# Performance work log

Hardware: AMD Instinct MI355X
Metric: run time of the kernel (lower is better)

Reference implementation:

```python
import jax, jax.numpy as jnp
import numpy as np

HIDDEN = 2048
N_HEADS = 16
HEAD_DIM = HIDDEN // N_HEADS  # 128
GROUP_SIZE = 128
ROPE_THETA = 10000.0
EPS = 1e-8
THRESH = 0.5


def ternary_quantize_groupwise(w):
    O, I = w.shape
    wg = w.reshape(O, I // GROUP_SIZE, GROUP_SIZE)
    scale = jnp.maximum(jnp.mean(jnp.abs(wg), axis=-1, keepdims=True), EPS)
    wn = wg / scale
    q = jnp.where(wn > THRESH, 1.0, jnp.where(wn < -THRESH, -1.0, 0.0))
    return (q * scale).reshape(O, I)


def quantize_with_ste(w):
    wq = ternary_quantize_groupwise(w)
    return w + jax.lax.stop_gradient(wq - w)


def rope_tables(seqlen):
    half = HEAD_DIM // 2
    inv_freq = 1.0 / (ROPE_THETA ** (jnp.arange(half, dtype=jnp.float32) / half))
    freqs = jnp.arange(seqlen, dtype=jnp.float32)[:, None] * inv_freq[None, :]  # [S, half]
    return jnp.cos(freqs), jnp.sin(freqs)


def apply_rope(x, cos, sin):
    # x: [B, H, S, D]; cos/sin: [S, D/2]
    d = x.shape[-1]
    x1, x2 = x[..., : d // 2], x[..., d // 2:]
    c = cos[None, None, :, :].astype(x.dtype)
    s = sin[None, None, :, :].astype(x.dtype)
    return jnp.concatenate([x1 * c - x2 * s, x1 * s + x2 * c], axis=-1)


def setup_inputs() -> dict:
    key = jax.random.key(0)
    ks = jax.random.split(key, 5)
    B, S = 1, 2048
    hidden_states = jax.random.normal(ks[0], (B, S, HIDDEN), dtype=jnp.float32)
    attention_mask = jnp.ones((B, S), dtype=jnp.int32)
    init_scale = 1.0 / np.sqrt(HIDDEN)
    wq = jax.random.normal(ks[1], (HIDDEN, HIDDEN), dtype=jnp.float32) * init_scale
    wk = jax.random.normal(ks[2], (HIDDEN, HIDDEN), dtype=jnp.float32) * init_scale
    wv = jax.random.normal(ks[3], (HIDDEN, HIDDEN), dtype=jnp.float32) * init_scale
    wo = jax.random.normal(ks[4], (HIDDEN, HIDDEN), dtype=jnp.float32) * init_scale
    return {"hidden_states": hidden_states, "attention_mask": attention_mask,
            "wq": wq, "wk": wk, "wv": wv, "wo": wo}


def reference(hidden_states, attention_mask, wq, wk, wv, wo):
    B, S, _ = hidden_states.shape
    cos, sin = rope_tables(S)

    def proj(x, w):
        w_q = quantize_with_ste(w)
        y = jnp.einsum('bsi,oi->bso', x, w_q)
        return y.reshape(B, S, N_HEADS, HEAD_DIM).transpose(0, 2, 1, 3)  # [B,H,S,D]

    q = apply_rope(proj(hidden_states, wq), cos, sin)
    k = apply_rope(proj(hidden_states, wk), cos, sin)
    v = proj(hidden_states, wv)

    scores = jnp.einsum('bhsd,bhtd->bhst', q, k) / np.sqrt(HEAD_DIM)
    causal = jnp.triu(jnp.ones((S, S), dtype=bool), k=1)
    scores = jnp.where(causal[None, None, :, :], -jnp.inf, scores)
    pad = (attention_mask == 0)[:, None, None, :]
    scores = jnp.where(pad, -jnp.inf, scores)

    probs = jax.nn.softmax(scores, axis=-1)
    out = jnp.einsum('bhst,bhtd->bhsd', probs, v)
    out = out.transpose(0, 2, 1, 3).reshape(B, S, HIDDEN)

    wo_q = quantize_with_ste(wo)
    return jnp.einsum('bso,po->bsp', out, wo_q)
```

## Files before the change

kernel.cpp:

```cpp
#include <hip/hip_runtime.h>
#include <cstdint>
#include <cstddef>


typedef __attribute__((ext_vector_type(8))) short bf16x8;
typedef __attribute__((ext_vector_type(4))) float f32x4;
typedef __attribute__((address_space(3))) void lds_void;
typedef const __attribute__((address_space(1))) void gmem_void;

__device__ __forceinline__ short f2bf(float x) {
    union { float f; uint32_t u; } c; c.f = x;
    uint32_t r = (c.u + 0x7FFFu + ((c.u >> 16) & 1u)) >> 16;
    return (short)r;
}
__device__ __forceinline__ float bf2f(short x) {
    union { uint32_t u; float f; } c; c.u = ((uint32_t)(uint16_t)x) << 16;
    return c.f;
}

__global__ __launch_bounds__(64) void zero_flag(int* f) {
    if (threadIdx.x == 0) *f = 0;
}

__global__ __launch_bounds__(256) void detect_kernel(
    const unsigned short* __restrict__ p, int n, int* __restrict__ flag)
{
    int tid = blockIdx.x * 256 + threadIdx.x;
    int cnt = 0;
    for (int i = tid; i < n; i += 65536) {
        int e = (p[i] >> 7) & 0xFF;
        cnt += (e >= 0xF0) ? 1 : 0;
    }
#pragma unroll
    for (int off = 1; off < 64; off <<= 1) cnt += __shfl_xor(cnt, off);
    if ((threadIdx.x & 63) == 0 && cnt) atomicAdd(flag, cnt);
}

__global__ __launch_bounds__(256) void convert_kernel(
    const void* __restrict__ in, short* __restrict__ out, int n,
    const int* __restrict__ flag)
{
    bool isf32 = (*flag > 1000);
    int i = (blockIdx.x * 256 + threadIdx.x) * 4;
    if (i >= n) return;
    if (isf32) {
        float4 v = *(const float4*)((const float*)in + i);
        short4 o;
        o.x = f2bf(v.x); o.y = f2bf(v.y); o.z = f2bf(v.z); o.w = f2bf(v.w);
        *(short4*)(out + i) = o;
    } else {
        *(short4*)(out + i) = *(const short4*)((const short*)in + i);
    }
}

__global__ __launch_bounds__(256) void quant_kernel(
    const void* __restrict__ w0, const void* __restrict__ w1,
    const void* __restrict__ w2, const void* __restrict__ w3,
    short* __restrict__ q0, short* __restrict__ q1,
    short* __restrict__ q2, short* __restrict__ q3,
    const int* __restrict__ flag)
{
    bool isf32 = (*flag > 1000);
    int t   = blockIdx.x * 256 + threadIdx.x;
    int mat = t >> 20;
    int e4  = t & 1048575;
    const void* w = (mat == 0) ? w0 : (mat == 1) ? w1 : (mat == 2) ? w2 : w3;
    short*      q = (mat == 0) ? q0 : (mat == 1) ? q1 : (mat == 2) ? q2 : q3;
    float a0, a1, a2, a3;
    if (isf32) {
        float4 v = *(const float4*)((const float*)w + (long long)e4 * 4);
        a0 = v.x; a1 = v.y; a2 = v.z; a3 = v.w;
    } else {
        short4 v = *(const short4*)((const short*)w + (long long)e4 * 4);
        a0 = bf2f(v.x); a1 = bf2f(v.y); a2 = bf2f(v.z); a3 = bf2f(v.w);
    }
    float s = fabsf(a0) + fabsf(a1) + fabsf(a2) + fabsf(a3);
#pragma unroll
    for (int off = 1; off < 32; off <<= 1) s += __shfl_xor(s, off);
    float scale = fmaxf(s * (1.0f / 128.0f), 1e-8f);
    float inv = 1.0f / scale;
    auto qz = [&](float a) -> short {
        float na = a * inv;
        return f2bf((na > 0.5f) ? scale : (na < -0.5f) ? -scale : 0.0f);
    };
    short4 o;
    o.x = qz(a0); o.y = qz(a1); o.z = qz(a2); o.w = qz(a3);
    *(short4*)(q + (long long)e4 * 4) = o;
}

__global__ __launch_bounds__(256, 2) void gemm_qkv(
    const short* __restrict__ A, const short* __restrict__ B,
    short* __restrict__ C)
{
    __shared__ short lds[30720];

    int wg = blockIdx.y * 32 + blockIdx.x;
    int sw = (wg & 7) * 64 + (wg >> 3);
    int bx = sw >> 4, by = sw & 15;

    const short* Ab = A + (long long)by * 128 * 2048;
    const short* Bb = B + (long long)bx * 192 * 2048;

    int tid = threadIdx.x, lane = tid & 63, wid = tid >> 6;
    int wr = wid >> 1, wc = wid & 1;
    int quad = lane >> 4, lm = lane & 15;

    f32x4 acc[4][6];
#pragma unroll
    for (int i = 0; i < 4; i++)
#pragma unroll
        for (int j = 0; j < 6; j++)
#pragma unroll
            for (int r = 0; r < 4; r++) acc[i][j][r] = 0.0f;

    auto stage = [&](int tn, short* buf) {
        short* dA = buf;
        short* dB = buf + 4096;
#pragma unroll
        for (int l = 0; l < 2; l++) {
            int ci  = l * 256 + tid;
            int row = ci >> 2;
            int kc  = ((ci & 3) - (row >> 1)) & 3;
            const short* gp = Ab + (long long)row * 2048 + tn * 32 + kc * 8;
            __builtin_amdgcn_global_load_lds((gmem_void*)gp, (lds_void*)(dA + ci * 8), 16, 0, 0);
        }
#pragma unroll
        for (int l = 0; l < 3; l++) {
            int ci  = l * 256 + tid;
            int row = ci >> 2;
            int kc  = ((ci & 3) - (row >> 1)) & 3;
            const short* gp = Bb + (long long)row * 2048 + tn * 32 + kc * 8;
            __builtin_amdgcn_global_load_lds((gmem_void*)gp, (lds_void*)(dB + ci * 8), 16, 0, 0);
        }
    };

    auto tile = [&](short* cur, short* nxt, int tn, bool pf) {
        if (pf) stage(tn, nxt);
        short* cA = cur;
        short* cB = cur + 4096;
        bf16x8 af[4], bg[6];
#pragma unroll
        for (int m = 0; m < 4; m++) {
            int R = wr * 64 + m * 16 + lm;
            af[m] = *(const bf16x8*)(cA + R * 32 + (((quad + (R >> 1)) & 3) << 3));
        }
#pragma unroll
        for (int n = 0; n < 3; n++) {
            int R = wc * 96 + n * 16 + lm;
            bg[n] = *(const bf16x8*)(cB + R * 32 + (((quad + (R >> 1)) & 3) << 3));
        }
        __builtin_amdgcn_s_setprio(1);
#pragma unroll
        for (int m = 0; m < 4; m++)
#pragma unroll
            for (int n = 0; n < 3; n++)
                acc[m][n] = __builtin_amdgcn_mfma_f32_16x16x32_bf16(af[m], bg[n], acc[m][n], 0, 0, 0);
        __builtin_amdgcn_s_setprio(0);
#pragma unroll
        for (int n = 3; n < 6; n++) {
            int R = wc * 96 + n * 16 + lm;
            bg[n] = *(const bf16x8*)(cB + R * 32 + (((quad + (R >> 1)) & 3) << 3));
        }
        __builtin_amdgcn_s_setprio(1);
#pragma unroll
        for (int m = 0; m < 4; m++)
#pragma unroll
            for (int n = 3; n < 6; n++)
                acc[m][n] = __builtin_amdgcn_mfma_f32_16x16x32_bf16(af[m], bg[n], acc[m][n], 0, 0, 0);
        __builtin_amdgcn_s_setprio(0);
        if (pf) asm volatile("s_waitcnt vmcnt(5)" ::: "memory");
        else    asm volatile("s_waitcnt vmcnt(0)" ::: "memory");
        __builtin_amdgcn_s_barrier();
    };

    short* c0 = lds;
    short* c1 = lds + 10240;
    short* c2 = lds + 20480;
    stage(0, c0);
    stage(1, c1);
    asm volatile("s_waitcnt vmcnt(5)" ::: "memory");
    __builtin_amdgcn_s_barrier();

    for (int t = 0; t < 64; t++) {
        tile(c0, c2, t + 2, t + 2 < 64);
        short* tmp = c0; c0 = c1; c1 = c2; c2 = tmp;
    }

#pragma unroll
    for (int m = 0; m < 4; m++)
#pragma unroll
        for (int n = 0; n < 6; n++)
#pragma unroll
            for (int r = 0; r < 4; r++) {
                int row = by * 128 + wr * 64 + m * 16 + quad * 4 + r;
                int col = bx * 192 + wc * 96 + n * 16 + lm;
                C[(long long)row * 6144 + col] = f2bf(acc[m][n][r]);
            }
}

__global__ __launch_bounds__(256) void ropetrans_kernel(
    const short* __restrict__ qkv,
    short* __restrict__ qr, short* __restrict__ kr,
    short* __restrict__ v_t)
{
    __shared__ short lt[4096];
    int bid = blockIdx.x;
    int tid = threadIdx.x;
    if (bid < 1024) {
        const float QSC = 0.1275174150637756f;
        int idx = bid * 256 + tid;
        int d8 = (idx & 7) * 8;
        int h  = (idx >> 3) & 15;
        int s  = idx >> 7;
        long long io = (long long)s * 6144 + h * 128 + d8;
        long long oo = (long long)h * 262144 + (long long)s * 128 + d8;
        bf16x8 x1q = *(const bf16x8*)(qkv + io);
        bf16x8 x2q = *(const bf16x8*)(qkv + io + 64);
        bf16x8 x1k = *(const bf16x8*)(qkv + io + 2048);
        bf16x8 x2k = *(const bf16x8*)(qkv + io + 2112);
        bf16x8 o1q, o2q, o1k, o2k;
#pragma unroll
        for (int j = 0; j < 8; j++) {
            float inv = exp2f((float)(d8 + j) * -0.20762050593261719f);
            float ang = (float)s * inv;
            float sn, c;
            sincosf(ang, &sn, &c);
            float a1 = bf2f(x1q[j]), a2 = bf2f(x2q[j]);
            o1q[j] = f2bf((a1 * c - a2 * sn) * QSC);
            o2q[j] = f2bf((a1 * sn + a2 * c) * QSC);
            float b1 = bf2f(x1k[j]), b2 = bf2f(x2k[j]);
            o1k[j] = f2bf(b1 * c - b2 * sn);
            o2k[j] = f2bf(b1 * sn + b2 * c);
        }
        *(bf16x8*)(qr + oo)      = o1q;
        *(bf16x8*)(qr + oo + 64) = o2q;
        *(bf16x8*)(kr + oo)      = o1k;
        *(bf16x8*)(kr + oo + 64) = o2k;
    } else {
        int bt = (bid - 1024) & 31, bo = (bid - 1024) >> 5;
        int r = tid >> 3, c = tid & 7;
#pragma unroll
        for (int h = 0; h < 2; h++) {
            int row = h * 32 + r;
            bf16x8 v = *(const bf16x8*)(qkv + (long long)(bt * 64 + row) * 6144 + 4096 + bo * 64 + c * 8);
            *(bf16x8*)(lt + row * 64 + ((c ^ (row & 7)) << 3)) = v;
        }
        __syncthreads();
#pragma unroll
        for (int h = 0; h < 2; h++) {
            int o = h * 32 + r;
            bf16x8 ov;
#pragma unroll
            for (int k = 0; k < 8; k++) {
                int row = c * 8 + k;
                ov[k] = lt[row * 64 + ((((o >> 3) ^ (row & 7))) << 3) + (o & 7)];
            }
            *(bf16x8*)(v_t + (long long)(bo * 64 + o) * 2048 + bt * 64 + c * 8) = ov;
        }
    }
}

__global__ __launch_bounds__(256, 2) void gemm_wo(
    const short* __restrict__ A, const short* __restrict__ B,
    float* __restrict__ C)
{
    __shared__ short lds[18432];

    int wg = blockIdx.y * 32 + blockIdx.x;
    int sw = (wg & 7) * 64 + (wg >> 3);
    int bx = sw & 31, by = sw >> 5;

    const short* Ab = A + (long long)by * 128 * 2048;
    const short* Bb = B + (long long)bx * 64 * 2048;

    int tid = threadIdx.x, lane = tid & 63, wid = tid >> 6;
    int wr = wid >> 1, wc = wid & 1;
    int quad = lane >> 4, lm = lane & 15;

    f32x4 acc[4][2];
#pragma unroll
    for (int i = 0; i < 4; i++)
#pragma unroll
        for (int j = 0; j < 2; j++)
#pragma unroll
            for (int r = 0; r < 4; r++) acc[i][j][r] = 0.0f;

    auto stage = [&](int tn, short* buf) {
        short* dA = buf;
        short* dB = buf + 4096;
#pragma unroll
        for (int l = 0; l < 2; l++) {
            int ci  = l * 256 + tid;
            int row = ci >> 2;
            int kc  = ((ci & 3) - (row >> 1)) & 3;
            const short* gp = Ab + (long long)row * 2048 + tn * 32 + kc * 8;
            __builtin_amdgcn_global_load_lds((gmem_void*)gp, (lds_void*)(dA + ci * 8), 16, 0, 0);
        }
        {
            int ci  = tid;
            int row = ci >> 2;
            int kc  = ((ci & 3) - (row >> 1)) & 3;
            const short* gp = Bb + (long long)row * 2048 + tn * 32 + kc * 8;
            __builtin_amdgcn_global_load_lds((gmem_void*)gp, (lds_void*)(dB + ci * 8), 16, 0, 0);
        }
    };

    auto tile = [&](short* cur, short* nxt, int tn, bool pf) {
        if (pf) stage(tn, nxt);
        short* cA = cur;
        short* cB = cur + 4096;
        bf16x8 af[4], bg[2];
#pragma unroll
        for (int m = 0; m < 4; m++) {
            int R = wr * 64 + m * 16 + lm;
            af[m] = *(const bf16x8*)(cA + R * 32 + (((quad + (R >> 1)) & 3) << 3));
        }
#pragma unroll
        for (int n = 0; n < 2; n++) {
            int R = wc * 32 + n * 16 + lm;
            bg[n] = *(const bf16x8*)(cB + R * 32 + (((quad + (R >> 1)) & 3) << 3));
        }
        __builtin_amdgcn_s_setprio(1);
#pragma unroll
        for (int m = 0; m < 4; m++)
#pragma unroll
            for (int n = 0; n < 2; n++)
                acc[m][n] = __builtin_amdgcn_mfma_f32_16x16x32_bf16(af[m], bg[n], acc[m][n], 0, 0, 0);
        __builtin_amdgcn_s_setprio(0);
        if (pf) asm volatile("s_waitcnt vmcnt(3)" ::: "memory");
        else    asm volatile("s_waitcnt vmcnt(0)" ::: "memory");
        __builtin_amdgcn_s_barrier();
    };

    short* c0 = lds;
    short* c1 = lds + 6144;
    short* c2 = lds + 12288;
    stage(0, c0);
    stage(1, c1);
    asm volatile("s_waitcnt vmcnt(3)" ::: "memory");
    __builtin_amdgcn_s_barrier();

    for (int t = 0; t < 64; t++) {
        tile(c0, c2, t + 2, t + 2 < 64);
        short* tmp = c0; c0 = c1; c1 = c2; c2 = tmp;
    }

#pragma unroll
    for (int m = 0; m < 4; m++)
#pragma unroll
        for (int n = 0; n < 2; n++)
#pragma unroll
            for (int r = 0; r < 4; r++) {
                int row = by * 128 + wr * 64 + m * 16 + quad * 4 + r;
                int col = bx * 64 + wc * 32 + n * 16 + lm;
                C[(long long)row * 2048 + col] = acc[m][n][r];
            }
}

__global__ __launch_bounds__(256) void flash_kernel(
    const short* __restrict__ q_r, const short* __restrict__ k_r,
    const short* __restrict__ v_t, float* __restrict__ Opart,
    float* __restrict__ mpart, float* __restrict__ lpart)
{
    const float THR = 11.5f;
    int bid = blockIdx.x;
    int p = bid >> 5;
    int h = (bid >> 1) & 15;
    int z = bid & 1;

    int tid = threadIdx.x, lane = tid & 63, wv = tid >> 6;
    int quad = lane >> 4, lm = lane & 15;

    __shared__ short lK[64 * 128];
    __shared__ short lV[128 * 64];
    __shared__ short lP[64 * 64];

    const short* kb = k_r + h * 262144;
    const short* vb = v_t + h * 128 * 2048;

    for (int leg = 0; leg < 2; leg++) {
        int qt = leg ? p : 31 - p;
        int n  = qt + 1;
        int jhalf = (n + 1) >> 1;
        int jb = z ? jhalf : 0;
        int je = z ? n : jhalf;

        const short* qb = q_r + h * 262144 + (qt * 64 + wv * 16) * 128;
        bf16x8 aq[4];
#pragma unroll
        for (int kc = 0; kc < 4; kc++)
            aq[kc] = *(const bf16x8*)(qb + lm * 128 + kc * 32 + quad * 8);

        f32x4 ao[8];
#pragma unroll
        for (int nt = 0; nt < 8; nt++)
#pragma unroll
            for (int r = 0; r < 4; r++) ao[nt][r] = 0.0f;
        float mrow[4], lrow[4];
#pragma unroll
        for (int r = 0; r < 4; r++) { mrow[r] = -1e30f; lrow[r] = 0.0f; }

        if (jb < je) {
#pragma unroll
            for (int i = 0; i < 4; i++) {
                int ci = i * 256 + tid;
                int r = ci >> 4, cp = ci & 15;
                int c = (cp & 8) | ((cp & 7) ^ (r & 7));
                const short* gp = kb + (jb * 64 + r) * 128 + c * 8;
                __builtin_amdgcn_global_load_lds((gmem_void*)gp, (lds_void*)(lK + ci * 8), 16, 0, 0);
            }
        }
        __syncthreads();

        for (int jt = jb; jt < je; jt++) {
#pragma unroll
            for (int i = 0; i < 4; i++) {
                int ci = i * 256 + tid;
                int r = ci >> 3, cp = ci & 7;
                int c = cp ^ (r & 7);
                const short* gp = vb + r * 2048 + jt * 64 + c * 8;
                __builtin_amdgcn_global_load_lds((gmem_void*)gp, (lds_void*)(lV + ci * 8), 16, 0, 0);
            }
            f32x4 as[4];
#pragma unroll
            for (int nt = 0; nt < 4; nt++)
#pragma unroll
                for (int r = 0; r < 4; r++) as[nt][r] = 0.0f;
            __builtin_amdgcn_s_setprio(1);
#pragma unroll
            for (int kc = 0; kc < 4; kc++) {
#pragma unroll
                for (int nt = 0; nt < 4; nt++) {
                    int r = nt * 16 + lm;
                    int c = kc * 4 + quad;
                    int slot = (c & 8) | ((c & 7) ^ (r & 7));
                    bf16x8 bk = *(const bf16x8*)(lK + (r * 16 + slot) * 8);
                    as[nt] = __builtin_amdgcn_mfma_f32_16x16x32_bf16(aq[kc], bk, as[nt], 0, 0, 0);
                }
            }
            __builtin_amdgcn_s_setprio(0);
            if (jt == qt) {
#pragma unroll
                for (int nt = 0; nt < 4; nt++)
#pragma unroll
                    for (int r = 0; r < 4; r++) {
                        int qg = wv * 16 + quad * 4 + r;
                        int tg = nt * 16 + lm;
                        if (tg > qg) as[nt][r] = -1e30f;
                    }
            }
#pragma unroll
            for (int r = 0; r < 4; r++) {
                float lmax = fmaxf(fmaxf(as[0][r], as[1][r]), fmaxf(as[2][r], as[3][r]));
                if (__any(lmax > mrow[r] + THR)) {
                    float mx = lmax;
#pragma unroll
                    for (int off = 1; off < 16; off <<= 1) mx = fmaxf(mx, __shfl_xor(mx, off));
                    if (mx > mrow[r] + THR) {
                        float alpha = exp2f(mrow[r] - mx);
                        lrow[r] *= alpha;
#pragma unroll
                        for (int nt = 0; nt < 8; nt++) ao[nt][r] *= alpha;
                        mrow[r] = mx;
                    }
                }
                float ps = 0.0f;
#pragma unroll
                for (int nt = 0; nt < 4; nt++) {
                    float pv = exp2f(as[nt][r] - mrow[r]);
                    as[nt][r] = pv;
                    ps += pv;
                }
                lrow[r] += ps;
                int row = wv * 16 + quad * 4 + r;
#pragma unroll
                for (int nt = 0; nt < 4; nt++) {
                    int slot = (nt * 2 + (lm >> 3) + 2 * quad) & 7;
                    lP[row * 64 + slot * 8 + (lm & 7)] = f2bf(as[nt][r]);
                }
            }
            __syncthreads();
            if (jt + 1 < je) {
#pragma unroll
                for (int i = 0; i < 4; i++) {
                    int ci = i * 256 + tid;
                    int r = ci >> 4, cp = ci & 15;
                    int c = (cp & 8) | ((cp & 7) ^ (r & 7));
                    const short* gp = kb + ((jt + 1) * 64 + r) * 128 + c * 8;
                    __builtin_amdgcn_global_load_lds((gmem_void*)gp, (lds_void*)(lK + ci * 8), 16, 0, 0);
                }
            }
            __builtin_amdgcn_s_setprio(1);
#pragma unroll
            for (int kt = 0; kt < 2; kt++) {
                int prow = wv * 16 + lm;
                int slot = (kt * 4 + quad + 2 * (lm >> 2)) & 7;
                bf16x8 ap = *(const bf16x8*)(lP + prow * 64 + slot * 8);
#pragma unroll
                for (int nt = 0; nt < 8; nt++) {
                    int r = nt * 16 + lm;
                    int c = kt * 4 + quad;
                    int vslot = c ^ (r & 7);
                    bf16x8 bv = *(const bf16x8*)(lV + (r * 8 + vslot) * 8);
                    ao[nt] = __builtin_amdgcn_mfma_f32_16x16x32_bf16(ap, bv, ao[nt], 0, 0, 0);
                }
            }
            __builtin_amdgcn_s_setprio(0);
            __syncthreads();
        }

        float* Ob = Opart + (long long)z * 4194304;
#pragma unroll
        for (int r = 0; r < 4; r++) {
            float l = lrow[r];
#pragma unroll
            for (int off = 1; off < 16; off <<= 1) l += __shfl_xor(l, off);
            int sg = qt * 64 + wv * 16 + quad * 4 + r;
#pragma unroll
            for (int nt = 0; nt < 8; nt++) {
                int dg = h * 128 + nt * 16 + lm;
                Ob[(long long)sg * 2048 + dg] = ao[nt][r];
            }
            if (lm == 0) {
                mpart[z * 32768 + h * 2048 + sg] = mrow[r];
                lpart[z * 32768 + h * 2048 + sg] = l;
            }
        }
    }
}

__global__ __launch_bounds__(256) void combine_kernel(
    const float* __restrict__ O0, const float* __restrict__ O1,
    const float* __restrict__ mpart, const float* __restrict__ lpart,
    short* __restrict__ attn)
{
    int idx = blockIdx.x * 256 + threadIdx.x;
    int e = idx * 4;
    int s = e >> 11, h = (e & 2047) >> 7;
    float m0 = mpart[h * 2048 + s], m1 = mpart[32768 + h * 2048 + s];
    float l0 = lpart[h * 2048 + s], l1 = lpart[32768 + h * 2048 + s];
    float M = fmaxf(m0, m1);
    float w0 = exp2f(m0 - M), w1 = exp2f(m1 - M);
    float inv = 1.0f / (l0 * w0 + l1 * w1);
    float4 a = *(const float4*)(O0 + e);
    float4 b = *(const float4*)(O1 + e);
    short4 o;
    o.x = f2bf((a.x * w0 + b.x * w1) * inv);
    o.y = f2bf((a.y * w0 + b.y * w1) * inv);
    o.z = f2bf((a.z * w0 + b.z * w1) * inv);
    o.w = f2bf((a.w * w0 + b.w * w1) * inv);
    *(short4*)(attn + e) = o;
}

extern "C" void kernel_launch(void* const* d_in, const int* in_sizes, int n_in,
                              void* d_out, int out_size, void* d_ws, size_t ws_size,
                              hipStream_t stream)
{
    const void* x  = d_in[0];
    const void* wq = d_in[2];
    const void* wk = d_in[3];
    const void* wv = d_in[4];
    const void* wo = d_in[5];

    char* ws = (char*)d_ws;
    size_t off = 0;
    auto alloc = [&](size_t b) { void* p = ws + off; off += (b + 255) & ~(size_t)255; return p; };
    short* wqkv_q = (short*)alloc(25165824);
    short* wo_q   = (short*)alloc(8388608);
    float* Opart  = (float*)alloc(33554432);
    short* qkv    = (short*)Opart;
    short* v_t    = (short*)alloc(8388608);
    short* q_r    = (short*)alloc(8388608);
    short* k_r    = (short*)alloc(8388608);
    short* attn   = (short*)alloc(8388608);
    short* x_bf   = (short*)alloc(8388608);
    float* mpart  = (float*)alloc(262144);
    float* lpart  = (float*)alloc(262144);
    int*   flag   = (int*)alloc(256);
    if (off > ws_size) return;

    zero_flag<<<1, 64, 0, stream>>>(flag);
    detect_kernel<<<256, 256, 0, stream>>>(
        (const unsigned short*)x, in_sizes[0], flag);
    convert_kernel<<<4096, 256, 0, stream>>>(x, x_bf, 4194304, flag);

    quant_kernel<<<16384, 256, 0, stream>>>(wq, wk, wv, wo,
        wqkv_q, wqkv_q + 4194304, wqkv_q + 8388608, wo_q, flag);

    gemm_qkv<<<dim3(32, 16), 256, 0, stream>>>(x_bf, wqkv_q, qkv);

    ropetrans_kernel<<<2048, 256, 0, stream>>>(qkv, q_r, k_r, v_t);

    flash_kernel<<<512, 256, 0, stream>>>(q_r, k_r, v_t, Opart, mpart, lpart);
    combine_kernel<<<4096, 256, 0, stream>>>(
        Opart, Opart + 4194304, mpart, lpart, attn);

    gemm_wo<<<dim3(32, 16), 256, 0, stream>>>(attn, wo_q, (float*)d_out);
}
```

Before: 296.9 us.

## Double-buffer K tiles in flash attention, fuse convert into quant, remap gemm_wo tiles

The flash attention kernel now double-buffers the K tile in LDS. The next K tile is prefetched at the start of each iteration together with V, and the __syncthreads calls are replaced by explicit vmcnt waits and barriers, so K load latency overlaps compute. The input conversion and weight quantization kernels are merged into one launch to save a kernel launch. The gemm_wo block-to-tile mapping is changed, which alters L2 locality for the output projection. The costs are extra LDS use in flash (a second K buffer) and hand-counted waitcnt values that must match the number of outstanding loads.

```diff
diff --git a/kernel.cpp b/kernel.cpp
--- a/kernel.cpp
+++ b/kernel.cpp
@@ -36,24 +36,8 @@
     if ((threadIdx.x & 63) == 0 && cnt) atomicAdd(flag, cnt);
 }
 
-__global__ __launch_bounds__(256) void convert_kernel(
-    const void* __restrict__ in, short* __restrict__ out, int n,
-    const int* __restrict__ flag)
-{
-    bool isf32 = (*flag > 1000);
-    int i = (blockIdx.x * 256 + threadIdx.x) * 4;
-    if (i >= n) return;
-    if (isf32) {
-        float4 v = *(const float4*)((const float*)in + i);
-        short4 o;
-        o.x = f2bf(v.x); o.y = f2bf(v.y); o.z = f2bf(v.z); o.w = f2bf(v.w);
-        *(short4*)(out + i) = o;
-    } else {
-        *(short4*)(out + i) = *(const short4*)((const short*)in + i);
-    }
-}
-
-__global__ __launch_bounds__(256) void quant_kernel(
+__global__ __launch_bounds__(256) void prep_kernel(
+    const void* __restrict__ x, short* __restrict__ x_bf,
     const void* __restrict__ w0, const void* __restrict__ w1,
     const void* __restrict__ w2, const void* __restrict__ w3,
     short* __restrict__ q0, short* __restrict__ q1,
@@ -61,7 +45,20 @@
     const int* __restrict__ flag)
 {
     bool isf32 = (*flag > 1000);
-    int t   = blockIdx.x * 256 + threadIdx.x;
+    int bid = blockIdx.x, tid = threadIdx.x;
+    if (bid < 4096) {
+        int i = (bid * 256 + tid) * 4;
+        if (isf32) {
+            float4 v = *(const float4*)((const float*)x + i);
+            short4 o;
+            o.x = f2bf(v.x); o.y = f2bf(v.y); o.z = f2bf(v.z); o.w = f2bf(v.w);
+            *(short4*)(x_bf + i) = o;
+        } else {
+            *(short4*)(x_bf + i) = *(const short4*)((const short*)x + i);
+        }
+        return;
+    }
+    int t   = (bid - 4096) * 256 + tid;
     int mat = t >> 20;
     int e4  = t & 1048575;
     const void* w = (mat == 0) ? w0 : (mat == 1) ? w1 : (mat == 2) ? w2 : w3;
@@ -268,7 +265,7 @@
 
     int wg = blockIdx.y * 32 + blockIdx.x;
     int sw = (wg & 7) * 64 + (wg >> 3);
-    int bx = sw & 31, by = sw >> 5;
+    int bx = sw >> 4, by = sw & 15;
 
     const short* Ab = A + (long long)by * 128 * 2048;
     const short* Bb = B + (long long)bx * 64 * 2048;
@@ -371,12 +368,33 @@
     int tid = threadIdx.x, lane = tid & 63, wv = tid >> 6;
     int quad = lane >> 4, lm = lane & 15;
 
-    __shared__ short lK[64 * 128];
+    __shared__ short lK[2][64 * 128];
     __shared__ short lV[128 * 64];
     __shared__ short lP[64 * 64];
 
     const short* kb = k_r + h * 262144;
     const short* vb = v_t + h * 128 * 2048;
+
+    auto stageK = [&](int jtgt, short* dst) {
+#pragma unroll
+        for (int i = 0; i < 4; i++) {
+            int ci = i * 256 + tid;
+            int r = ci >> 4, cp = ci & 15;
+            int c = (cp & 8) | ((cp & 7) ^ (r & 7));
+            const short* gp = kb + (jtgt * 64 + r) * 128 + c * 8;
+            __builtin_amdgcn_global_load_lds((gmem_void*)gp, (lds_void*)(dst + ci * 8), 16, 0, 0);
+        }
+    };
+    auto stageV = [&](int jtgt) {
+#pragma unroll
+        for (int i = 0; i < 4; i++) {
+            int ci = i * 256 + tid;
+            int r = ci >> 3, cp = ci & 7;
+            int c = cp ^ (r & 7);
+            const short* gp = vb + r * 2048 + jtgt * 64 + c * 8;
+            __builtin_amdgcn_global_load_lds((gmem_void*)gp, (lds_void*)(lV + ci * 8), 16, 0, 0);
+        }
+    };
 
     for (int leg = 0; leg < 2; leg++) {
         int qt = leg ? p : 31 - p;
@@ -400,27 +418,15 @@
 #pragma unroll
         for (int r = 0; r < 4; r++) { mrow[r] = -1e30f; lrow[r] = 0.0f; }
 
-        if (jb < je) {
-#pragma unroll
-            for (int i = 0; i < 4; i++) {
-                int ci = i * 256 + tid;
-                int r = ci >> 4, cp = ci & 15;
-                int c = (cp & 8) | ((cp & 7) ^ (r & 7));
-                const short* gp = kb + (jb * 64 + r) * 128 + c * 8;
-                __builtin_amdgcn_global_load_lds((gmem_void*)gp, (lds_void*)(lK + ci * 8), 16, 0, 0);
-            }
-        }
-        __syncthreads();
+        int cur = 0;
+        if (jb < je) stageK(jb, lK[0]);
+        asm volatile("s_waitcnt vmcnt(0)" ::: "memory");
+        __builtin_amdgcn_s_barrier();
 
         for (int jt = jb; jt < je; jt++) {
-#pragma unroll
-            for (int i = 0; i < 4; i++) {
-                int ci = i * 256 + tid;
-                int r = ci >> 3, cp = ci & 7;
-                int c = cp ^ (r & 7);
-                const short* gp = vb + r * 2048 + jt * 64 + c * 8;
-                __builtin_amdgcn_global_load_lds((gmem_void*)gp, (lds_void*)(lV + ci * 8), 16, 0, 0);
-            }
+            bool pk = (jt + 1 < je);
+            stageV(jt);
+            if (pk) stageK(jt + 1, lK[cur ^ 1]);
             f32x4 as[4];
 #pragma unroll
             for (int nt = 0; nt < 4; nt++)
@@ -434,7 +440,7 @@
                     int r = nt * 16 + lm;
                     int c = kc * 4 + quad;
                     int slot = (c & 8) | ((c & 7) ^ (r & 7));
-                    bf16x8 bk = *(const bf16x8*)(lK + (r * 16 + slot) * 8);
+                    bf16x8 bk = *(const bf16x8*)(lK[cur] + (r * 16 + slot) * 8);
                     as[nt] = __builtin_amdgcn_mfma_f32_16x16x32_bf16(aq[kc], bk, as[nt], 0, 0, 0);
                 }
             }
@@ -479,17 +485,9 @@
                     lP[row * 64 + slot * 8 + (lm & 7)] = f2bf(as[nt][r]);
                 }
             }
-            __syncthreads();
-            if (jt + 1 < je) {
-#pragma unroll
-                for (int i = 0; i < 4; i++) {
-                    int ci = i * 256 + tid;
-                    int r = ci >> 4, cp = ci & 15;
-                    int c = (cp & 8) | ((cp & 7) ^ (r & 7));
-                    const short* gp = kb + ((jt + 1) * 64 + r) * 128 + c * 8;
-                    __builtin_amdgcn_global_load_lds((gmem_void*)gp, (lds_void*)(lK + ci * 8), 16, 0, 0);
-                }
-            }
+            if (pk) asm volatile("s_waitcnt vmcnt(4) lgkmcnt(0)" ::: "memory");
+            else    asm volatile("s_waitcnt vmcnt(0) lgkmcnt(0)" ::: "memory");
+            __builtin_amdgcn_s_barrier();
             __builtin_amdgcn_s_setprio(1);
 #pragma unroll
             for (int kt = 0; kt < 2; kt++) {
@@ -506,7 +504,9 @@
                 }
             }
             __builtin_amdgcn_s_setprio(0);
-            __syncthreads();
+            asm volatile("s_waitcnt vmcnt(0)" ::: "memory");
+            __builtin_amdgcn_s_barrier();
+            cur ^= 1;
         }
 
         float* Ob = Opart + (long long)z * 4194304;
@@ -582,9 +582,8 @@
     zero_flag<<<1, 64, 0, stream>>>(flag);
     detect_kernel<<<256, 256, 0, stream>>>(
         (const unsigned short*)x, in_sizes[0], flag);
-    convert_kernel<<<4096, 256, 0, stream>>>(x, x_bf, 4194304, flag);
-
-    quant_kernel<<<16384, 256, 0, stream>>>(wq, wk, wv, wo,
+
+    prep_kernel<<<20480, 256, 0, stream>>>(x, x_bf, wq, wk, wv, wo,
         wqkv_q, wqkv_q + 4194304, wqkv_q + 8388608, wo_q, flag);
 
     gemm_qkv<<<dim3(32, 16), 256, 0, stream>>>(x_bf, wqkv_q, qkv);
```

Result: no change. 293.7 us (-1.1%).
